# Performance work log

Measured on AMD Instinct MI355X. Metric: run time of the kernel, lower is better.

The kernel has to match this reference:

```python
import jax, jax.numpy as jnp
from jax import lax
import numpy as np

HPDF = np.array([-0.0544158422, 0.3128715909, -0.6756307363, 0.5853546837,
                 0.0158291053, -0.284015543, -0.0004724846, 0.1287474266,
                 0.017369301, -0.0440882539, -0.0139810279, 0.008746094,
                 0.004870353, -0.0003917404, -0.0006754494, -0.0001174768],
                dtype=np.float32)


def setup_inputs() -> dict:
    key = jax.random.key(0)
    x = jax.random.normal(key, (8, 3, 512, 512), dtype=jnp.float32)
    hpdf = jnp.asarray(HPDF)
    return {"x": x, "hpdf": hpdf}


def _dwconv(inp, k2d, channels):
    # depthwise valid cross-correlation (matches F.conv2d with groups=C)
    n = k2d.shape[0]
    k = jnp.broadcast_to(k2d[None, None], (channels, 1, n, n))
    return lax.conv_general_dilated(
        inp, k, window_strides=(1, 1), padding='VALID',
        dimension_numbers=('NCHW', 'OIHW', 'NCHW'),
        feature_group_count=channels)


def reference(x, hpdf):
    B, C, H, W = x.shape
    n = hpdf.shape[0]  # 16 taps
    sign = (-1.0) ** jnp.arange(n, dtype=jnp.float32)
    lpdf = sign * hpdf[::-1]
    filters = [jnp.outer(lpdf, hpdf),   # LH
               jnp.outer(hpdf, lpdf),   # HL
               jnp.outer(hpdf, hpdf)]   # HH
    pad = n - 1  # 15
    xp = jnp.pad(x, ((0, 0), (0, 0), (pad, pad), (pad, pad)), mode='reflect')

    xis = []
    for f in filters:
        R = _dwconv(xp, f, C)                       # [B,C,H+15,W+15]
        xi = _dwconv(jnp.abs(R), jnp.abs(f[::-1, ::-1]), C)  # [B,C,H,W]
        # filter side length 16 is even -> roll by 1 on both spatial dims
        xi = jnp.roll(jnp.roll(xi, 1, axis=-1), 1, axis=-2)
        xis.append(xi)

    xi_stack = jnp.stack(xis, axis=0)               # [3,B,C,H,W]
    # p = -1: rho = (sum xi^p)^(-1/p) = sum(1/xi)
    rho = jnp.sum(1.0 / xi_stack, axis=0)
    wet = 1e10
    rho = jnp.minimum(rho, wet)
    rho = jnp.where(jnp.isnan(rho), wet, rho)
    mn = rho.min(axis=(-2, -1), keepdims=True)
    mx = rho.max(axis=(-2, -1), keepdims=True)
    rho = (rho - mn) / (mx - mn + 1e-8)
    score = jax.nn.sigmoid(1.0 - rho)
    return x * score
```

## Files before the change

### kernel.cpp

```cpp
#include <hip/hip_runtime.h>
#include <math.h>

#define IMG   512
#define NIMG  24
#define XST   72
#define TST   104
#define RST   56
#define UST   88

#define SA_TL  0
#define SA_TH  4992
#define SA_X   9984
#define SA_R   9984
#define RSZ    4480
#define SA_U   0
#define USZ    2816
#define SA_FT  22112
#define POOLSZ 23424

typedef _Float16 v8h __attribute__((ext_vector_type(8)));
typedef float    v4f __attribute__((ext_vector_type(4)));

__device__ __forceinline__ v8h load8(const _Float16* p) {
    union { uint4 u; v8h h; } c;
    c.u = *(const uint4*)p;
    return c.h;
}

__device__ __forceinline__ unsigned pkrtz(float a, float b) {
    union { __fp16 __attribute__((ext_vector_type(2))) v; unsigned u; } c;
    c.v = __builtin_amdgcn_cvt_pkrtz(a, b);
    return c.u;
}

__device__ __forceinline__ void store4(_Float16* p, v4f a) {
    union { _Float16 h[4]; uint2 u; } c;
    c.h[0] = (_Float16)a[0]; c.h[1] = (_Float16)a[1];
    c.h[2] = (_Float16)a[2]; c.h[3] = (_Float16)a[3];
    *(uint2*)p = c.u;
}

__device__ __forceinline__ void store4abs(_Float16* p, v4f a) {
    union { _Float16 h[4]; uint2 u; } c;
    c.h[0] = (_Float16)fabsf(a[0]); c.h[1] = (_Float16)fabsf(a[1]);
    c.h[2] = (_Float16)fabsf(a[2]); c.h[3] = (_Float16)fabsf(a[3]);
    *(uint2*)p = c.u;
}

__device__ __forceinline__ unsigned short f2bf(float f) {
    unsigned b = __float_as_uint(f);
    b = (b + 0x7fffu + ((b >> 16) & 1u)) >> 16;
    return (unsigned short)b;
}

__device__ __forceinline__ int refl(int g) {
    return g < 0 ? -g : (g >= IMG ? 2 * IMG - 2 - g : g);
}

__global__ __launch_bounds__(512, 6) void stego_stage1(
    const float* __restrict__ x, const float* __restrict__ hpdf,
    unsigned short* __restrict__ rho_out, float2* __restrict__ bmm)
{
    __shared__ __align__(16) _Float16 pool[POOLSZ];
    __shared__ float red[16];

    const int tid = threadIdx.x;
    const int lane = tid & 63;
    const int wid = __builtin_amdgcn_readfirstlane(tid >> 6);
    const int n16 = lane & 15, quad = lane >> 4;

    const int blk = blockIdx.x;
    const int xcd = blk & 7;
    const int grp = blk >> 3;
    const int img = xcd + ((grp >> 7) << 3);
    const int tl  = grp & 127;
    const int Oi = (tl >> 4) << 6;
    const int Oj = (tl & 15) << 5;
    const float* ximg = x + (size_t)img * (IMG * IMG);

    for (int e = tid; e < 1312; e += 512) {
        const int mode = e >> 3 == 0 ? 0 : (e / 328);
        const int rem  = e - mode * 328;
        const int tap  = (rem >> 3) + (rem & 7) - 16;
        float v = 0.f;
        if (tap >= 0 && tap <= 15) {
            int idx = (mode == 0 || mode == 2) ? tap : 15 - tap;
            float c = hpdf[idx];
            if (mode == 1 && (tap & 1)) c = -c;
            if (mode >= 2) c = fabsf(c);
            v = c;
        }
        pool[SA_FT + e] = (_Float16)v;
    }

    {
        const int cg = tid & 15, row0 = tid >> 4;
        const int c0 = Oj - 16 + 4 * cg;
        _Float16* dst = pool + SA_X + row0 * XST + 4 * cg;
        if (Oi >= 15 && Oi <= 433 && Oj >= 16 && Oj <= 464) {
            const float* src = ximg + (size_t)(Oi - 15 + row0) * IMG + c0;
            #pragma unroll
            for (int k = 0; k < 3; ++k) {
                const int row = row0 + (k << 5);
                uint2 pv = make_uint2(0u, 0u);
                if (row < 94) {
                    float4 xv = *(const float4*)(src + (size_t)(k << 5) * IMG);
                    pv.x = pkrtz(xv.x, xv.y);
                    pv.y = pkrtz(xv.z, xv.w);
                }
                *(uint2*)(dst + (size_t)(k << 5) * XST) = pv;
            }
        } else {
            const int gj0 = refl(c0),     gj1 = refl(c0 + 1);
            const int gj2 = refl(c0 + 2), gj3 = refl(c0 + 3);
            #pragma unroll
            for (int k = 0; k < 3; ++k) {
                const int row = row0 + (k << 5);
                uint2 pv = make_uint2(0u, 0u);
                if (row < 94) {
                    const float* rsrc = ximg + (size_t)refl(Oi - 15 + row) * IMG;
                    pv.x = pkrtz(rsrc[gj0], rsrc[gj1]);
                    pv.y = pkrtz(rsrc[gj2], rsrc[gj3]);
                }
                *(uint2*)(dst + (size_t)(k << 5) * XST) = pv;
            }
        }
    }
    __syncthreads();

    v8h band[4], bandA[2];
    {
        const int sA = 16 + quad * 8 - n16;
        #pragma unroll
        for (int m = 0; m < 4; ++m)
            band[m] = load8(pool + SA_FT + (m * 41 + sA) * 8);
        #pragma unroll
        for (int m = 0; m < 2; ++m)
            bandA[m] = load8(pool + SA_FT + (m * 41 + sA - 1) * 8);
    }

    for (int u = wid; u < 18; u += 8) {
        int mt = u % 6, nt = u / 6;
        int m0 = mt * 16, n0 = nt * 16;
        v8h a = load8(pool + SA_X + (m0 + n16) * XST + n0 + quad * 8);
        v4f z = {0.f, 0.f, 0.f, 0.f};
        v4f cL = __builtin_amdgcn_mfma_f32_16x16x32_f16(a, bandA[1], z, 0, 0, 0);
        v4f cH = __builtin_amdgcn_mfma_f32_16x16x32_f16(a, bandA[0], z, 0, 0, 0);
        int off = (n0 + n16) * TST + m0 + quad * 4;
        store4(pool + SA_TL + off, cL);
        store4(pool + SA_TH + off, cH);
    }
    __syncthreads();

    float rho[4] = {0.f, 0.f, 0.f, 0.f};
    const int fB[3] = {0, 1, 0};
    const int fC[3] = {2, 3, 3};
    const int fD[3] = {3, 2, 3};

    #pragma unroll
    for (int f = 0; f < 3; ++f) {
        const _Float16* Tsrc = pool + (f == 0 ? SA_TL : SA_TH);
        _Float16* Rf = pool + SA_R + f * RSZ;
        for (int u = wid; u < 15; u += 8) {
            int nt = u % 5, mt = u / 5;
            int i0 = nt * 16, c0 = mt * 16;
            v8h a = load8(Tsrc + (c0 + n16) * TST + i0 + quad * 8);
            v4f z = {0.f, 0.f, 0.f, 0.f};
            v4f acc = __builtin_amdgcn_mfma_f32_16x16x32_f16(a, band[fB[f]], z, 0, 0, 0);
            store4abs(Rf + (i0 + n16) * RST + c0 + quad * 4, acc);
        }
    }
    __syncthreads();

    #pragma unroll
    for (int f = 0; f < 3; ++f) {
        const _Float16* Rf = pool + SA_R + f * RSZ;
        _Float16* Uf = pool + SA_U + f * USZ;
        for (int u = wid; u < 10; u += 8) {
            int mt = u % 5, nt = u / 5;
            int i0 = mt * 16, j0 = nt * 16;
            v8h a = load8(Rf + (i0 + n16) * RST + j0 + quad * 8);
            v4f z = {0.f, 0.f, 0.f, 0.f};
            v4f acc = __builtin_amdgcn_mfma_f32_16x16x32_f16(a, band[fC[f]], z, 0, 0, 0);
            store4(Uf + (j0 + n16) * UST + i0 + quad * 4, acc);
        }
    }
    __syncthreads();

    {
        const int i0 = (wid & 3) * 16, c0 = (wid >> 2) * 16;
        #pragma unroll
        for (int f = 0; f < 3; ++f) {
            const _Float16* Uf = pool + SA_U + f * USZ;
            v8h a = load8(Uf + (c0 + n16) * UST + i0 + quad * 8);
            v4f z = {0.f, 0.f, 0.f, 0.f};
            v4f acc = __builtin_amdgcn_mfma_f32_16x16x32_f16(a, band[fD[f]], z, 0, 0, 0);
            #pragma unroll
            for (int r = 0; r < 4; ++r) rho[r] += __builtin_amdgcn_rcpf(acc[r]);
        }
    }

    const size_t rbase = (size_t)img * (IMG * IMG);
    const int i_nat = Oi + (wid & 3) * 16 + n16;
    const int jb = Oj + ((wid >> 2) << 4) + quad * 4;
    float lmin = 1e38f, lmax = 0.f;
    unsigned pk0, pk1;
    {
        unsigned short b[4];
        #pragma unroll
        for (int r = 0; r < 4; ++r) {
            float v = rho[r];
            v = isnan(v) ? 1e10f : fminf(v, 1e10f);
            b[r] = f2bf(v);
            float rq = __uint_as_float((unsigned)b[r] << 16);
            lmin = fminf(lmin, rq);
            lmax = fmaxf(lmax, rq);
        }
        pk0 = (unsigned)b[0] | ((unsigned)b[1] << 16);
        pk1 = (unsigned)b[2] | ((unsigned)b[3] << 16);
    }
    *(uint2*)(rho_out + rbase + ((size_t)i_nat << 9) + jb) = make_uint2(pk0, pk1);

    #pragma unroll
    for (int off = 32; off >= 1; off >>= 1) {
        lmin = fminf(lmin, __shfl_xor(lmin, off));
        lmax = fmaxf(lmax, __shfl_xor(lmax, off));
    }
    if ((tid & 63) == 0) { red[wid] = lmin; red[8 + wid] = lmax; }
    __syncthreads();
    if (tid == 0) {
        float m0 = red[0], m1 = red[8];
        #pragma unroll
        for (int k = 1; k < 8; ++k) { m0 = fminf(m0, red[k]); m1 = fmaxf(m1, red[8 + k]); }
        bmm[(img << 7) + tl] = make_float2(m0, m1);
    }
}

__global__ __launch_bounds__(256) void stego_stage2(
    const float* __restrict__ x, const unsigned short* __restrict__ rho,
    const float2* __restrict__ bmm, float* __restrict__ out)
{
    __shared__ float sred[8];
    const int tid = threadIdx.x;
    const int lane = tid & 63;

    const int blk = blockIdx.x;
    const int xcd = blk & 7, grp = blk >> 3;
    const int img = xcd + ((grp >> 7) << 3);
    const int chunk = grp & 127;
    const int t = (img << 15) + (chunk << 8) + tid;

    float lmn = 1e38f, lmx = 0.f;
    if (tid < 128) { float2 p = bmm[(img << 7) + tid]; lmn = p.x; lmx = p.y; }
    #pragma unroll
    for (int off = 32; off >= 1; off >>= 1) {
        lmn = fminf(lmn, __shfl_xor(lmn, off));
        lmx = fmaxf(lmx, __shfl_xor(lmx, off));
    }
    if (tid < 128 && (tid & 63) == 0) { sred[tid >> 6] = lmn; sred[4 + (tid >> 6)] = lmx; }
    __syncthreads();
    const float mn = fminf(sred[0], sred[1]);
    const float mx = fmaxf(sred[4], sred[5]);
    const float inv = __builtin_amdgcn_rcpf(mx - mn + 1e-8f);

    const int i = (t >> 6) & 511;
    const int rrow = (i - 1) & 511;
    const size_t rb_off = ((size_t)img << 18) + ((size_t)rrow << 9) + ((size_t)lane << 3);
    uint4 rb = *(const uint4*)(rho + rb_off);
    unsigned ru[4] = {rb.x, rb.y, rb.z, rb.w};
    float f7 = __uint_as_float(ru[3] & 0xffff0000u);
    float r[8];
    r[0] = __shfl(f7, (lane + 63) & 63);
    r[1] = __uint_as_float(ru[0] << 16);
    r[2] = __uint_as_float(ru[0] & 0xffff0000u);
    r[3] = __uint_as_float(ru[1] << 16);
    r[4] = __uint_as_float(ru[1] & 0xffff0000u);
    r[5] = __uint_as_float(ru[2] << 16);
    r[6] = __uint_as_float(ru[2] & 0xffff0000u);
    r[7] = __uint_as_float(ru[3] << 16);

    const size_t base = (size_t)t << 3;
    const float* xrow = x + base;
    float4 xa = *(const float4*)xrow;
    float4 xb = *(const float4*)(xrow + 4);
    float xs[8] = {xa.x, xa.y, xa.z, xa.w, xb.x, xb.y, xb.z, xb.w};
    float os[8];
    #pragma unroll
    for (int k = 0; k < 8; ++k) {
        float rn = (r[k] - mn) * inv;
        os[k] = xs[k] * __builtin_amdgcn_rcpf(1.f + __expf(rn - 1.f));
    }
    float* orow = out + base;
    *(float4*)orow       = make_float4(os[0], os[1], os[2], os[3]);
    *(float4*)(orow + 4) = make_float4(os[4], os[5], os[6], os[7]);
}

extern "C" void kernel_launch(void* const* d_in, const int* in_sizes, int n_in,
                              void* d_out, int out_size, void* d_ws, size_t ws_size,
                              hipStream_t stream) {
    const float* x    = (const float*)d_in[0];
    const float* hpdf = (const float*)d_in[1];
    float* out = (float*)d_out;

    unsigned short* rho = (unsigned short*)d_ws;
    float2* bmm = (float2*)((char*)d_ws + (size_t)NIMG * IMG * IMG * 2);

    hipLaunchKernelGGL(stego_stage1, dim3(NIMG * 128), dim3(512), 0, stream,
                       x, hpdf, rho, bmm);
    hipLaunchKernelGGL(stego_stage2, dim3(NIMG * 128), dim3(256), 0, stream,
                       x, rho, bmm, out);
}
```

Baseline: 108.6 us.

## Enlarge stage-1 output tiles to 64x64 to cut halo recompute

Stage 1 now computes 64x64 output tiles instead of 64x32. The larger tile lowers the share of work spent on the 15-pixel halo in the input staging and in the separable MFMA passes. The grid is halved, and every shared-memory buffer is widened, which pushes the pool from about 47 KB to about 79 KB. Occupancy drops from 6 to 4 blocks per CU. Work-unit assignment is rotated across waves per filter to balance the uneven tile counts, and stage 2 reduces 64 min/max partials per image instead of 128.

```diff
diff --git a/kernel.cpp b/kernel.cpp
--- a/kernel.cpp
+++ b/kernel.cpp
@@ -3,20 +3,20 @@
 
 #define IMG   512
 #define NIMG  24
-#define XST   72
+#define XST   104
 #define TST   104
-#define RST   56
+#define RST   88
 #define UST   88
 
 #define SA_TL  0
-#define SA_TH  4992
-#define SA_X   9984
-#define SA_R   9984
-#define RSZ    4480
+#define SA_TH  8320
+#define SA_X   16896
+#define SA_R   16896
+#define RSZ    7040
 #define SA_U   0
-#define USZ    2816
-#define SA_FT  22112
-#define POOLSZ 23424
+#define USZ    5632
+#define SA_FT  38016
+#define POOLSZ 39328
 
 typedef _Float16 v8h __attribute__((ext_vector_type(8)));
 typedef float    v4f __attribute__((ext_vector_type(4)));
@@ -57,7 +57,7 @@
     return g < 0 ? -g : (g >= IMG ? 2 * IMG - 2 - g : g);
 }
 
-__global__ __launch_bounds__(512, 6) void stego_stage1(
+__global__ __launch_bounds__(512, 4) void stego_stage1(
     const float* __restrict__ x, const float* __restrict__ hpdf,
     unsigned short* __restrict__ rho_out, float2* __restrict__ bmm)
 {
@@ -72,14 +72,14 @@
     const int blk = blockIdx.x;
     const int xcd = blk & 7;
     const int grp = blk >> 3;
-    const int img = xcd + ((grp >> 7) << 3);
-    const int tl  = grp & 127;
-    const int Oi = (tl >> 4) << 6;
-    const int Oj = (tl & 15) << 5;
+    const int img = xcd + ((grp >> 6) << 3);
+    const int tl  = grp & 63;
+    const int Oi = (tl >> 3) << 6;
+    const int Oj = (tl & 7) << 6;
     const float* ximg = x + (size_t)img * (IMG * IMG);
 
     for (int e = tid; e < 1312; e += 512) {
-        const int mode = e >> 3 == 0 ? 0 : (e / 328);
+        const int mode = e / 328;
         const int rem  = e - mode * 328;
         const int tap  = (rem >> 3) + (rem & 7) - 16;
         float v = 0.f;
@@ -93,37 +93,29 @@
         pool[SA_FT + e] = (_Float16)v;
     }
 
-    {
-        const int cg = tid & 15, row0 = tid >> 4;
-        const int c0 = Oj - 16 + 4 * cg;
-        _Float16* dst = pool + SA_X + row0 * XST + 4 * cg;
-        if (Oi >= 15 && Oi <= 433 && Oj >= 16 && Oj <= 464) {
-            const float* src = ximg + (size_t)(Oi - 15 + row0) * IMG + c0;
-            #pragma unroll
-            for (int k = 0; k < 3; ++k) {
-                const int row = row0 + (k << 5);
-                uint2 pv = make_uint2(0u, 0u);
-                if (row < 94) {
-                    float4 xv = *(const float4*)(src + (size_t)(k << 5) * IMG);
-                    pv.x = pkrtz(xv.x, xv.y);
-                    pv.y = pkrtz(xv.z, xv.w);
-                }
-                *(uint2*)(dst + (size_t)(k << 5) * XST) = pv;
+    if (Oi >= 15 && Oi <= 433 && Oj >= 16 && Oj <= 432) {
+        const float* src = ximg + (size_t)(Oi - 15) * IMG + (Oj - 16);
+        for (int p = tid; p < 2304; p += 512) {
+            const int row = p / 24, cg = p - row * 24;
+            uint2 pv = make_uint2(0u, 0u);
+            if (row < 94) {
+                float4 xv = *(const float4*)(src + (size_t)row * IMG + 4 * cg);
+                pv.x = pkrtz(xv.x, xv.y);
+                pv.y = pkrtz(xv.z, xv.w);
             }
-        } else {
-            const int gj0 = refl(c0),     gj1 = refl(c0 + 1);
-            const int gj2 = refl(c0 + 2), gj3 = refl(c0 + 3);
-            #pragma unroll
-            for (int k = 0; k < 3; ++k) {
-                const int row = row0 + (k << 5);
-                uint2 pv = make_uint2(0u, 0u);
-                if (row < 94) {
-                    const float* rsrc = ximg + (size_t)refl(Oi - 15 + row) * IMG;
-                    pv.x = pkrtz(rsrc[gj0], rsrc[gj1]);
-                    pv.y = pkrtz(rsrc[gj2], rsrc[gj3]);
-                }
-                *(uint2*)(dst + (size_t)(k << 5) * XST) = pv;
+            *(uint2*)(pool + SA_X + row * XST + 4 * cg) = pv;
+        }
+    } else {
+        for (int p = tid; p < 2304; p += 512) {
+            const int row = p / 24, cg = p - row * 24;
+            uint2 pv = make_uint2(0u, 0u);
+            if (row < 94) {
+                const float* rsrc = ximg + (size_t)refl(Oi - 15 + row) * IMG;
+                const int c0 = Oj - 16 + 4 * cg;
+                pv.x = pkrtz(rsrc[refl(c0)],     rsrc[refl(c0 + 1)]);
+                pv.y = pkrtz(rsrc[refl(c0 + 2)], rsrc[refl(c0 + 3)]);
             }
+            *(uint2*)(pool + SA_X + row * XST + 4 * cg) = pv;
         }
     }
     __syncthreads();
@@ -139,7 +131,7 @@
             bandA[m] = load8(pool + SA_FT + (m * 41 + sA - 1) * 8);
     }
 
-    for (int u = wid; u < 18; u += 8) {
+    for (int u = wid; u < 30; u += 8) {
         int mt = u % 6, nt = u / 6;
         int m0 = mt * 16, n0 = nt * 16;
         v8h a = load8(pool + SA_X + (m0 + n16) * XST + n0 + quad * 8);
@@ -152,16 +144,18 @@
     }
     __syncthreads();
 
-    float rho[4] = {0.f, 0.f, 0.f, 0.f};
+    float rho[2][4] = {{0.f, 0.f, 0.f, 0.f}, {0.f, 0.f, 0.f, 0.f}};
     const int fB[3] = {0, 1, 0};
     const int fC[3] = {2, 3, 3};
     const int fD[3] = {3, 2, 3};
+    const int rotB[3] = {0, 3, 6};
+    const int rotC[3] = {0, 4, 2};
 
     #pragma unroll
     for (int f = 0; f < 3; ++f) {
         const _Float16* Tsrc = pool + (f == 0 ? SA_TL : SA_TH);
         _Float16* Rf = pool + SA_R + f * RSZ;
-        for (int u = wid; u < 15; u += 8) {
+        for (int u = (wid + rotB[f]) & 7; u < 25; u += 8) {
             int nt = u % 5, mt = u / 5;
             int i0 = nt * 16, c0 = mt * 16;
             v8h a = load8(Tsrc + (c0 + n16) * TST + i0 + quad * 8);
@@ -176,7 +170,7 @@
     for (int f = 0; f < 3; ++f) {
         const _Float16* Rf = pool + SA_R + f * RSZ;
         _Float16* Uf = pool + SA_U + f * USZ;
-        for (int u = wid; u < 10; u += 8) {
+        for (int u = (wid + rotC[f]) & 7; u < 20; u += 8) {
             int mt = u % 5, nt = u / 5;
             int i0 = mt * 16, j0 = nt * 16;
             v8h a = load8(Rf + (i0 + n16) * RST + j0 + quad * 8);
@@ -187,8 +181,10 @@
     }
     __syncthreads();
 
-    {
-        const int i0 = (wid & 3) * 16, c0 = (wid >> 2) * 16;
+    #pragma unroll
+    for (int s = 0; s < 2; ++s) {
+        const int v = 2 * wid + s;
+        const int i0 = (v & 3) << 4, c0 = (v >> 2) << 4;
         #pragma unroll
         for (int f = 0; f < 3; ++f) {
             const _Float16* Uf = pool + SA_U + f * USZ;
@@ -196,30 +192,31 @@
             v4f z = {0.f, 0.f, 0.f, 0.f};
             v4f acc = __builtin_amdgcn_mfma_f32_16x16x32_f16(a, band[fD[f]], z, 0, 0, 0);
             #pragma unroll
-            for (int r = 0; r < 4; ++r) rho[r] += __builtin_amdgcn_rcpf(acc[r]);
+            for (int r = 0; r < 4; ++r) rho[s][r] += __builtin_amdgcn_rcpf(acc[r]);
         }
     }
 
     const size_t rbase = (size_t)img * (IMG * IMG);
-    const int i_nat = Oi + (wid & 3) * 16 + n16;
-    const int jb = Oj + ((wid >> 2) << 4) + quad * 4;
     float lmin = 1e38f, lmax = 0.f;
-    unsigned pk0, pk1;
-    {
+    #pragma unroll
+    for (int s = 0; s < 2; ++s) {
+        const int v = 2 * wid + s;
+        const int i_nat = Oi + ((v & 3) << 4) + n16;
+        const int jb = Oj + ((v >> 2) << 4) + quad * 4;
         unsigned short b[4];
         #pragma unroll
         for (int r = 0; r < 4; ++r) {
-            float v = rho[r];
-            v = isnan(v) ? 1e10f : fminf(v, 1e10f);
-            b[r] = f2bf(v);
+            float w = rho[s][r];
+            w = isnan(w) ? 1e10f : fminf(w, 1e10f);
+            b[r] = f2bf(w);
             float rq = __uint_as_float((unsigned)b[r] << 16);
             lmin = fminf(lmin, rq);
             lmax = fmaxf(lmax, rq);
         }
-        pk0 = (unsigned)b[0] | ((unsigned)b[1] << 16);
-        pk1 = (unsigned)b[2] | ((unsigned)b[3] << 16);
-    }
-    *(uint2*)(rho_out + rbase + ((size_t)i_nat << 9) + jb) = make_uint2(pk0, pk1);
+        unsigned pk0 = (unsigned)b[0] | ((unsigned)b[1] << 16);
+        unsigned pk1 = (unsigned)b[2] | ((unsigned)b[3] << 16);
+        *(uint2*)(rho_out + rbase + ((size_t)i_nat << 9) + jb) = make_uint2(pk0, pk1);
+    }
 
     #pragma unroll
     for (int off = 32; off >= 1; off >>= 1) {
@@ -232,7 +229,7 @@
         float m0 = red[0], m1 = red[8];
         #pragma unroll
         for (int k = 1; k < 8; ++k) { m0 = fminf(m0, red[k]); m1 = fmaxf(m1, red[8 + k]); }
-        bmm[(img << 7) + tl] = make_float2(m0, m1);
+        bmm[(img << 6) + tl] = make_float2(m0, m1);
     }
 }
 
@@ -240,7 +237,7 @@
     const float* __restrict__ x, const unsigned short* __restrict__ rho,
     const float2* __restrict__ bmm, float* __restrict__ out)
 {
-    __shared__ float sred[8];
+    __shared__ float sred[2];
     const int tid = threadIdx.x;
     const int lane = tid & 63;
 
@@ -250,17 +247,19 @@
     const int chunk = grp & 127;
     const int t = (img << 15) + (chunk << 8) + tid;
 
-    float lmn = 1e38f, lmx = 0.f;
-    if (tid < 128) { float2 p = bmm[(img << 7) + tid]; lmn = p.x; lmx = p.y; }
-    #pragma unroll
-    for (int off = 32; off >= 1; off >>= 1) {
-        lmn = fminf(lmn, __shfl_xor(lmn, off));
-        lmx = fmaxf(lmx, __shfl_xor(lmx, off));
-    }
-    if (tid < 128 && (tid & 63) == 0) { sred[tid >> 6] = lmn; sred[4 + (tid >> 6)] = lmx; }
-    __syncthreads();
-    const float mn = fminf(sred[0], sred[1]);
-    const float mx = fmaxf(sred[4], sred[5]);
+    if (tid < 64) {
+        float2 p = bmm[(img << 6) + tid];
+        float lmn = p.x, lmx = p.y;
+        #pragma unroll
+        for (int off = 32; off >= 1; off >>= 1) {
+            lmn = fminf(lmn, __shfl_xor(lmn, off));
+            lmx = fmaxf(lmx, __shfl_xor(lmx, off));
+        }
+        if (tid == 0) { sred[0] = lmn; sred[1] = lmx; }
+    }
+    __syncthreads();
+    const float mn = sred[0];
+    const float mx = sred[1];
     const float inv = __builtin_amdgcn_rcpf(mx - mn + 1e-8f);
 
     const int i = (t >> 6) & 511;
@@ -305,7 +304,7 @@
     unsigned short* rho = (unsigned short*)d_ws;
     float2* bmm = (float2*)((char*)d_ws + (size_t)NIMG * IMG * IMG * 2);
 
-    hipLaunchKernelGGL(stego_stage1, dim3(NIMG * 128), dim3(512), 0, stream,
+    hipLaunchKernelGGL(stego_stage1, dim3(NIMG * 64), dim3(512), 0, stream,
                        x, hpdf, rho, bmm);
     hipLaunchKernelGGL(stego_stage2, dim3(NIMG * 128), dim3(256), 0, stream,
                        x, rho, bmm, out);
```

After: 109.4 us. No clear change (+0.8%).

## Load input directly into MFMA operands and alias LDS buffers to shrink pool

Applied to the files above, without the earlier changes.

The input tile is no longer staged through shared memory. Each wave loads and converts its rows straight from global memory into the MFMA A operand. The LDS pool is reorganised so the R and U intermediate buffers alias one another across extra barrier-separated phases, which cuts LDS per block and lets launch bounds rise from 6 to 8 blocks. The cost is more __syncthreads phases with serialised stages, plus uncoalesced per-wave global loads in place of cooperative staging.

```diff
diff --git a/kernel.cpp b/kernel.cpp
--- a/kernel.cpp
+++ b/kernel.cpp
@@ -3,20 +3,20 @@
 
 #define IMG   512
 #define NIMG  24
-#define XST   72
 #define TST   104
 #define RST   56
 #define UST   88
 
 #define SA_TL  0
 #define SA_TH  4992
-#define SA_X   9984
-#define SA_R   9984
-#define RSZ    4480
-#define SA_U   0
-#define USZ    2816
-#define SA_FT  22112
-#define POOLSZ 23424
+#define SA_R0  9984
+#define SA_R1  0
+#define SA_R2  14464
+#define SA_U0  4992
+#define SA_U1  9984
+#define SA_U2  0
+#define SA_FT  14464
+#define POOLSZ 18944
 
 typedef _Float16 v8h __attribute__((ext_vector_type(8)));
 typedef float    v4f __attribute__((ext_vector_type(4)));
@@ -57,7 +57,7 @@
     return g < 0 ? -g : (g >= IMG ? 2 * IMG - 2 - g : g);
 }
 
-__global__ __launch_bounds__(512, 6) void stego_stage1(
+__global__ __launch_bounds__(512, 8) void stego_stage1(
     const float* __restrict__ x, const float* __restrict__ hpdf,
     unsigned short* __restrict__ rho_out, float2* __restrict__ bmm)
 {
@@ -77,9 +77,10 @@
     const int Oi = (tl >> 4) << 6;
     const int Oj = (tl & 15) << 5;
     const float* ximg = x + (size_t)img * (IMG * IMG);
+    const bool interior = (Oi >= 15 && Oi <= 433 && Oj >= 16 && Oj <= 464);
 
     for (int e = tid; e < 1312; e += 512) {
-        const int mode = e >> 3 == 0 ? 0 : (e / 328);
+        const int mode = e / 328;
         const int rem  = e - mode * 328;
         const int tap  = (rem >> 3) + (rem & 7) - 16;
         float v = 0.f;
@@ -92,40 +93,6 @@
         }
         pool[SA_FT + e] = (_Float16)v;
     }
-
-    {
-        const int cg = tid & 15, row0 = tid >> 4;
-        const int c0 = Oj - 16 + 4 * cg;
-        _Float16* dst = pool + SA_X + row0 * XST + 4 * cg;
-        if (Oi >= 15 && Oi <= 433 && Oj >= 16 && Oj <= 464) {
-            const float* src = ximg + (size_t)(Oi - 15 + row0) * IMG + c0;
-            #pragma unroll
-            for (int k = 0; k < 3; ++k) {
-                const int row = row0 + (k << 5);
-                uint2 pv = make_uint2(0u, 0u);
-                if (row < 94) {
-                    float4 xv = *(const float4*)(src + (size_t)(k << 5) * IMG);
-                    pv.x = pkrtz(xv.x, xv.y);
-                    pv.y = pkrtz(xv.z, xv.w);
-                }
-                *(uint2*)(dst + (size_t)(k << 5) * XST) = pv;
-            }
-        } else {
-            const int gj0 = refl(c0),     gj1 = refl(c0 + 1);
-            const int gj2 = refl(c0 + 2), gj3 = refl(c0 + 3);
-            #pragma unroll
-            for (int k = 0; k < 3; ++k) {
-                const int row = row0 + (k << 5);
-                uint2 pv = make_uint2(0u, 0u);
-                if (row < 94) {
-                    const float* rsrc = ximg + (size_t)refl(Oi - 15 + row) * IMG;
-                    pv.x = pkrtz(rsrc[gj0], rsrc[gj1]);
-                    pv.y = pkrtz(rsrc[gj2], rsrc[gj3]);
-                }
-                *(uint2*)(dst + (size_t)(k << 5) * XST) = pv;
-            }
-        }
-    }
     __syncthreads();
 
     v8h band[4], bandA[2];
@@ -139,65 +106,96 @@
             bandA[m] = load8(pool + SA_FT + (m * 41 + sA - 1) * 8);
     }
 
+    const v4f z = {0.f, 0.f, 0.f, 0.f};
+
     for (int u = wid; u < 18; u += 8) {
-        int mt = u % 6, nt = u / 6;
-        int m0 = mt * 16, n0 = nt * 16;
-        v8h a = load8(pool + SA_X + (m0 + n16) * XST + n0 + quad * 8);
-        v4f z = {0.f, 0.f, 0.f, 0.f};
-        v4f cL = __builtin_amdgcn_mfma_f32_16x16x32_f16(a, bandA[1], z, 0, 0, 0);
-        v4f cH = __builtin_amdgcn_mfma_f32_16x16x32_f16(a, bandA[0], z, 0, 0, 0);
-        int off = (n0 + n16) * TST + m0 + quad * 4;
+        const int mt = u % 6, nt = u / 6;
+        const int m0 = mt * 16, n0 = nt * 16;
+        const int row = m0 + n16;
+        union { unsigned uu[4]; v8h h; } cc;
+        cc.uu[0] = cc.uu[1] = cc.uu[2] = cc.uu[3] = 0u;
+        if (row < 94) {
+            const int gcol = Oj - 16 + n0 + quad * 8;
+            if (interior) {
+                const float* rp = ximg + (size_t)(Oi - 15 + row) * IMG + gcol;
+                float4 xa = *(const float4*)rp;
+                float4 xb = *(const float4*)(rp + 4);
+                cc.uu[0] = pkrtz(xa.x, xa.y); cc.uu[1] = pkrtz(xa.z, xa.w);
+                cc.uu[2] = pkrtz(xb.x, xb.y); cc.uu[3] = pkrtz(xb.z, xb.w);
+            } else {
+                const float* rsrc = ximg + (size_t)refl(Oi - 15 + row) * IMG;
+                float xv[8];
+                #pragma unroll
+                for (int e = 0; e < 8; ++e) xv[e] = rsrc[refl(gcol + e)];
+                cc.uu[0] = pkrtz(xv[0], xv[1]); cc.uu[1] = pkrtz(xv[2], xv[3]);
+                cc.uu[2] = pkrtz(xv[4], xv[5]); cc.uu[3] = pkrtz(xv[6], xv[7]);
+            }
+        }
+        v4f cL = __builtin_amdgcn_mfma_f32_16x16x32_f16(cc.h, bandA[1], z, 0, 0, 0);
+        v4f cH = __builtin_amdgcn_mfma_f32_16x16x32_f16(cc.h, bandA[0], z, 0, 0, 0);
+        const int off = (n0 + n16) * TST + m0 + quad * 4;
         store4(pool + SA_TL + off, cL);
         store4(pool + SA_TH + off, cH);
     }
     __syncthreads();
 
-    float rho[4] = {0.f, 0.f, 0.f, 0.f};
-    const int fB[3] = {0, 1, 0};
-    const int fC[3] = {2, 3, 3};
-    const int fD[3] = {3, 2, 3};
-
-    #pragma unroll
-    for (int f = 0; f < 3; ++f) {
-        const _Float16* Tsrc = pool + (f == 0 ? SA_TL : SA_TH);
-        _Float16* Rf = pool + SA_R + f * RSZ;
-        for (int u = wid; u < 15; u += 8) {
-            int nt = u % 5, mt = u / 5;
-            int i0 = nt * 16, c0 = mt * 16;
-            v8h a = load8(Tsrc + (c0 + n16) * TST + i0 + quad * 8);
-            v4f z = {0.f, 0.f, 0.f, 0.f};
-            v4f acc = __builtin_amdgcn_mfma_f32_16x16x32_f16(a, band[fB[f]], z, 0, 0, 0);
-            store4abs(Rf + (i0 + n16) * RST + c0 + quad * 4, acc);
-        }
-    }
-    __syncthreads();
-
-    #pragma unroll
-    for (int f = 0; f < 3; ++f) {
-        const _Float16* Rf = pool + SA_R + f * RSZ;
-        _Float16* Uf = pool + SA_U + f * USZ;
-        for (int u = wid; u < 10; u += 8) {
-            int mt = u % 5, nt = u / 5;
-            int i0 = mt * 16, j0 = nt * 16;
-            v8h a = load8(Rf + (i0 + n16) * RST + j0 + quad * 8);
-            v4f z = {0.f, 0.f, 0.f, 0.f};
-            v4f acc = __builtin_amdgcn_mfma_f32_16x16x32_f16(a, band[fC[f]], z, 0, 0, 0);
-            store4(Uf + (j0 + n16) * UST + i0 + quad * 4, acc);
-        }
-    }
-    __syncthreads();
-
+    for (int u = wid; u < 15; u += 8) {
+        const int i0 = (u % 5) * 16, c0 = (u / 5) * 16;
+        v8h a = load8(pool + SA_TL + (c0 + n16) * TST + i0 + quad * 8);
+        v4f acc = __builtin_amdgcn_mfma_f32_16x16x32_f16(a, band[0], z, 0, 0, 0);
+        store4abs(pool + SA_R0 + (i0 + n16) * RST + c0 + quad * 4, acc);
+    }
+    __syncthreads();
+
+    for (int v = wid; v < 30; v += 8) {
+        const int hi = v >= 15;
+        const int rem = hi ? v - 15 : v;
+        const int i0 = (rem % 5) * 16, c0 = (rem / 5) * 16;
+        v8h a = load8(pool + SA_TH + (c0 + n16) * TST + i0 + quad * 8);
+        v4f acc = __builtin_amdgcn_mfma_f32_16x16x32_f16(
+            a, hi ? band[0] : band[1], z, 0, 0, 0);
+        store4abs(pool + (hi ? SA_R2 : SA_R1) + (i0 + n16) * RST + c0 + quad * 4, acc);
+    }
+    __syncthreads();
+
+    for (int u = wid; u < 10; u += 8) {
+        const int i0 = (u % 5) * 16, j0 = (u / 5) * 16;
+        v8h a = load8(pool + SA_R0 + (i0 + n16) * RST + j0 + quad * 8);
+        v4f acc = __builtin_amdgcn_mfma_f32_16x16x32_f16(a, band[2], z, 0, 0, 0);
+        store4(pool + SA_U0 + (j0 + n16) * UST + i0 + quad * 4, acc);
+    }
+    __syncthreads();
+
+    for (int u = wid; u < 10; u += 8) {
+        const int i0 = (u % 5) * 16, j0 = (u / 5) * 16;
+        v8h a = load8(pool + SA_R1 + (i0 + n16) * RST + j0 + quad * 8);
+        v4f acc = __builtin_amdgcn_mfma_f32_16x16x32_f16(a, band[3], z, 0, 0, 0);
+        store4(pool + SA_U1 + (j0 + n16) * UST + i0 + quad * 4, acc);
+    }
+    __syncthreads();
+
+    for (int u = wid; u < 10; u += 8) {
+        const int i0 = (u % 5) * 16, j0 = (u / 5) * 16;
+        v8h a = load8(pool + SA_R2 + (i0 + n16) * RST + j0 + quad * 8);
+        v4f acc = __builtin_amdgcn_mfma_f32_16x16x32_f16(a, band[3], z, 0, 0, 0);
+        store4(pool + SA_U2 + (j0 + n16) * UST + i0 + quad * 4, acc);
+    }
+    __syncthreads();
+
+    float rho[4];
     {
         const int i0 = (wid & 3) * 16, c0 = (wid >> 2) * 16;
-        #pragma unroll
-        for (int f = 0; f < 3; ++f) {
-            const _Float16* Uf = pool + SA_U + f * USZ;
-            v8h a = load8(Uf + (c0 + n16) * UST + i0 + quad * 8);
-            v4f z = {0.f, 0.f, 0.f, 0.f};
-            v4f acc = __builtin_amdgcn_mfma_f32_16x16x32_f16(a, band[fD[f]], z, 0, 0, 0);
-            #pragma unroll
-            for (int r = 0; r < 4; ++r) rho[r] += __builtin_amdgcn_rcpf(acc[r]);
-        }
+        const int ub = (c0 + n16) * UST + i0 + quad * 8;
+        v8h d0 = load8(pool + SA_U0 + ub);
+        v8h d1 = load8(pool + SA_U1 + ub);
+        v8h d2 = load8(pool + SA_U2 + ub);
+        v4f x0 = __builtin_amdgcn_mfma_f32_16x16x32_f16(d0, band[3], z, 0, 0, 0);
+        v4f x1 = __builtin_amdgcn_mfma_f32_16x16x32_f16(d1, band[2], z, 0, 0, 0);
+        v4f x2 = __builtin_amdgcn_mfma_f32_16x16x32_f16(d2, band[3], z, 0, 0, 0);
+        #pragma unroll
+        for (int r = 0; r < 4; ++r)
+            rho[r] = __builtin_amdgcn_rcpf(x0[r]) + __builtin_amdgcn_rcpf(x1[r])
+                   + __builtin_amdgcn_rcpf(x2[r]);
     }
 
     const size_t rbase = (size_t)img * (IMG * IMG);
```

Result: slower. 123.1 us (+13.4%).
